# Optimization experiments

Measured on AMD Instinct MI355X. Metric: run time of the kernel, lower is better.

The kernel has to match this reference:

```python
import jax, jax.numpy as jnp
import numpy as np

BN_EPS = 1e-5

def _gin_mlp(h, wa, ba, wb, bb):
    # 2-layer MLP: Linear -> ReLU -> Linear
    return jax.nn.relu(h @ wa + ba) @ wb + bb

def _gin_conv(x, src, dst, n, wa, ba, wb, bb):
    # GIN aggregation: (1+eps)*x + sum_{j->i} x_j, eps=0 (PyG default)
    agg = jax.ops.segment_sum(x[src], dst, num_segments=n)
    return _gin_mlp(x + agg, wa, ba, wb, bb)

def _batchnorm(h, gamma, beta):
    # track_running_stats=False -> always batch stats, biased variance
    mean = jnp.mean(h, axis=0)
    var = jnp.var(h, axis=0)
    return (h - mean) * jax.lax.rsqrt(var + BN_EPS) * gamma + beta

def setup_inputs() -> dict:
    key = jax.random.key(0)
    ks = jax.random.split(key, 8)
    N, E, F, H, C = 100000, 1600000, 64, 64, 10
    s = 0.05
    return {
        "x": jax.random.normal(ks[0], (N, F), dtype=jnp.float32),
        "edge_index": jax.random.randint(ks[1], (2, E), 0, N, dtype=jnp.int64),
        "w1a": jax.random.normal(ks[2], (F, H), dtype=jnp.float32) * s,
        "b1a": jnp.zeros((H,), jnp.float32),
        "w1b": jax.random.normal(ks[3], (H, H), dtype=jnp.float32) * s,
        "b1b": jnp.zeros((H,), jnp.float32),
        "bn_gamma": jnp.ones((H,), jnp.float32),
        "bn_beta": jnp.zeros((H,), jnp.float32),
        "w2a": jax.random.normal(ks[4], (H, H), dtype=jnp.float32) * s,
        "b2a": jnp.zeros((H,), jnp.float32),
        "w2b": jax.random.normal(ks[5], (H, H), dtype=jnp.float32) * s,
        "b2b": jnp.zeros((H,), jnp.float32),
        "lin_w": jax.random.normal(ks[6], (H, C), dtype=jnp.float32) * s,
        "lin_b": jnp.zeros((C,), jnp.float32),
    }

def reference(x, edge_index, w1a, b1a, w1b, b1b, bn_gamma, bn_beta,
              w2a, b2a, w2b, b2b, lin_w, lin_b):
    n = x.shape[0]
    src, dst = edge_index[0], edge_index[1]
    h1 = _gin_conv(x, src, dst, n, w1a, b1a, w1b, b1b)   # [N, H]
    h1 = _batchnorm(h1, bn_gamma, bn_beta)               # relu1 never applied (faithful)
    h2 = _gin_conv(h1, src, dst, n, w2a, b2a, w2b, b2b)  # [N, H]
    return h2 @ lin_w + lin_b                            # [N, C]
```

## Files before the change

kernel.cpp:

```cpp
#include <hip/hip_runtime.h>
#include <hip/hip_fp16.h>

#define H 64
#define CBS 512
#define CB_BITS 9
#define TILE 8192
#define CAP 9216
#define NSTAT 64
#define RPK_BLKS 53

typedef _Float16 f16;
typedef __attribute__((ext_vector_type(8))) _Float16 v8h;
typedef __attribute__((ext_vector_type(4))) float v4f;

__global__ __launch_bounds__(256)
void init_kernel(int* __restrict__ gcursor, float* __restrict__ statsR, int CB) {
    int t = threadIdx.x;
    if (t < CB) gcursor[t * 16] = t * CAP;
    for (int i = t; i < NSTAT * 128; i += 256) statsR[i] = 0.f;
}

__global__ __launch_bounds__(256)
void front_kernel(const int* __restrict__ ei, int* __restrict__ gcursor,
                  int* __restrict__ pairs, int E, int N, int CB, int ntiles,
                  const float* __restrict__ x, f16* __restrict__ xh, int total4,
                  const float* __restrict__ W1a, const float* __restrict__ W1b,
                  const float* __restrict__ W2a, const float* __restrict__ W2b,
                  const float* __restrict__ B2b, const float* __restrict__ LW,
                  const float* __restrict__ LB,
                  f16* __restrict__ pk1a, f16* __restrict__ pk1b,
                  f16* __restrict__ pk2a, f16* __restrict__ pkf,
                  float* __restrict__ bf) {
    __shared__ int sd[256];
    __shared__ int excl[256];
    __shared__ int gbase[256];
    __shared__ int lcur[256];
    __shared__ int stage[TILE];
    __shared__ unsigned char bin8[TILE];
    int b = blockIdx.x;
    int t = threadIdx.x;

    if (b < ntiles) {
        int base = b * TILE;
        int cnt = min(TILE, E - base);
        sd[t] = 0;
        __syncthreads();
        for (int i = t; i < cnt; i += 256) {
            int s = ei[base + i];
            int d = ei[E + base + i];
            if ((unsigned)s < (unsigned)N && (unsigned)d < (unsigned)N)
                atomicAdd(&sd[d >> CB_BITS], 1);
        }
        __syncthreads();
        int v = sd[t];
        __syncthreads();
        for (int off = 1; off < 256; off <<= 1) {
            int add = (t >= off) ? sd[t - off] : 0;
            __syncthreads();
            sd[t] += add;
            __syncthreads();
        }
        int ex = sd[t] - v;
        excl[t] = ex;
        lcur[t] = ex;
        if (t < CB && v > 0) gbase[t] = atomicAdd(&gcursor[t * 16], v);
        int tot = sd[255];
        __syncthreads();
        for (int i = t; i < cnt; i += 256) {
            int s = ei[base + i];
            int d = ei[E + base + i];
            if ((unsigned)s < (unsigned)N && (unsigned)d < (unsigned)N) {
                int cb = d >> CB_BITS;
                int pos = atomicAdd(&lcur[cb], 1);
                stage[pos] = s | ((d & (CBS - 1)) << 17);
                bin8[pos] = (unsigned char)cb;
            }
        }
        __syncthreads();
        for (int i = t; i < tot; i += 256) {
            int b8 = bin8[i];
            pairs[gbase[b8] + (i - excl[b8])] = stage[i];
        }
        return;
    }
    b -= ntiles;
    if (b < RPK_BLKS) {
        int tt = b * 256 + t;
        if (tt < 12288) {
            int m = tt >> 12;
            int e = tt & 4095;
            int j = e & 7, lane = (e >> 3) & 63, ks = (e >> 9) & 1, nt = e >> 10;
            int row = ks * 32 + ((lane >> 4) & 3) * 8 + j;
            int col = nt * 16 + (lane & 15);
            const float* W = (m == 0) ? W1a : (m == 1) ? W1b : W2a;
            f16* P = (m == 0) ? pk1a : (m == 1) ? pk1b : pk2a;
            P[e] = (f16)W[row * 64 + col];
        } else if (tt < 13312) {
            int e = tt - 12288;
            int j = e & 7, lane = (e >> 3) & 63, ks = e >> 9;
            int row = ks * 32 + ((lane >> 4) & 3) * 8 + j;
            int col = lane & 15;
            float a = 0.f;
            if (col < 10)
                for (int m = 0; m < H; ++m) a = fmaf(W2b[row * 64 + m], LW[m * 10 + col], a);
            pkf[e] = (f16)a;
        } else if (tt < 13322) {
            int c = tt - 13312;
            float a = LB[c];
            for (int m = 0; m < H; ++m) a = fmaf(B2b[m], LW[m * 10 + c], a);
            bf[c] = a;
        }
        return;
    }
    b -= RPK_BLKS;
    int i = b * 256 + t;
    if (i >= total4) return;
    float4 v = ((const float4*)x)[i];
    f16 h0 = (f16)v.x, h1 = (f16)v.y, h2 = (f16)v.z, h3 = (f16)v.w;
    ushort4 pk;
    pk.x = *(unsigned short*)&h0; pk.y = *(unsigned short*)&h1;
    pk.z = *(unsigned short*)&h2; pk.w = *(unsigned short*)&h3;
    ((ushort4*)xh)[i] = pk;
}

__global__ __launch_bounds__(256)
void bucket_csr_kernel(const int* __restrict__ pairs, const int* __restrict__ gcursor,
                       int* __restrict__ ebuf, int* __restrict__ rowptr, int N, int CB) {
    __shared__ int hist[CBS];
    __shared__ int cur[CBS];
    __shared__ int sd[256];
    __shared__ int carry_s;
    int b = blockIdx.x;
    int t = threadIdx.x;
    int c_t = (t < CB) ? (gcursor[t * 16] - t * CAP) : 0;
    sd[t] = c_t; __syncthreads();
    for (int off = 1; off < 256; off <<= 1) {
        int add = (t >= off) ? sd[t - off] : 0;
        __syncthreads();
        sd[t] += add;
        __syncthreads();
    }
    int cnt = gcursor[b * 16] - b * CAP;
    int gb = sd[b] - cnt;
    if (b == 0 && t == 0) rowptr[N] = sd[255];
    __syncthreads();

    int pb = b * CAP;
    for (int i = t; i < CBS; i += 256) hist[i] = 0;
    if (t == 0) carry_s = 0;
    __syncthreads();
    for (int i = t; i < cnt; i += 256)
        atomicAdd(&hist[(pairs[pb + i] >> 17) & (CBS - 1)], 1);
    __syncthreads();
    for (int start = 0; start < CBS; start += 256) {
        int v = hist[start + t];
        sd[t] = v; __syncthreads();
        for (int off = 1; off < 256; off <<= 1) {
            int add = (t >= off) ? sd[t - off] : 0;
            __syncthreads();
            sd[t] += add;
            __syncthreads();
        }
        int ex = sd[t] - v + carry_s;
        cur[start + t] = ex;
        int node = b * CBS + start + t;
        if (node < N) rowptr[node] = gb + ex;
        __syncthreads();
        if (t == 0) carry_s += sd[255];
        __syncthreads();
    }
    for (int i = t; i < cnt; i += 256) {
        int p = pairs[pb + i];
        int pos = atomicAdd(&cur[(p >> 17) & (CBS - 1)], 1);
        ebuf[gb + pos] = p & 0x1FFFF;
    }
}

__global__ __launch_bounds__(256)
void gather1_kernel(const f16* __restrict__ xh, const int* __restrict__ rowptr,
                    const int* __restrict__ ebuf, f16* __restrict__ bufA,
                    int N, int Em1) {
    int wid = (int)(((long long)blockIdx.x * blockDim.x + threadIdx.x) >> 6);
    int lane = threadIdx.x & 63;
    int g = lane >> 3, fl = lane & 7;
    int node = wid * 8 + g;
    bool vn = node < N;
    int p0 = 0, deg = 0;
    if (vn) {
        p0 = rowptr[node];
        deg = rowptr[node + 1] - p0;
    }
    float a[8];
    {
        v8h s = {};
        if (vn) s = *(const v8h*)(xh + ((size_t)node << 6) + fl * 8);
#pragma unroll
        for (int j = 0; j < 8; ++j) a[j] = (float)s[j];
    }
    int k = 0;
    for (; k + 8 <= deg; k += 8) {
        int idx[8];
#pragma unroll
        for (int q = 0; q < 8; ++q) idx[q] = ebuf[p0 + k + q];
#pragma unroll
        for (int q = 0; q < 8; ++q) {
            v8h v = *(const v8h*)(xh + ((size_t)idx[q] << 6) + fl * 8);
#pragma unroll
            for (int j = 0; j < 8; ++j) a[j] += (float)v[j];
        }
    }
    if (k < deg) {
        int idx[8];
#pragma unroll
        for (int q = 0; q < 8; ++q) idx[q] = ebuf[min(p0 + k + q, Em1)];
#pragma unroll
        for (int q = 0; q < 8; ++q) {
            if (k + q < deg) {
                v8h v = *(const v8h*)(xh + ((size_t)idx[q] << 6) + fl * 8);
#pragma unroll
                for (int j = 0; j < 8; ++j) a[j] += (float)v[j];
            }
        }
    }
    if (vn) {
        v8h o;
#pragma unroll
        for (int j = 0; j < 8; ++j) o[j] = (f16)a[j];
        *(v8h*)(bufA + ((size_t)node << 6) + fl * 8) = o;
    }
}

__global__ __launch_bounds__(256)
void gather2_kernel(const f16* __restrict__ h1p, const float* __restrict__ scale,
                    const float* __restrict__ shiftv, const int* __restrict__ rowptr,
                    const int* __restrict__ ebuf, f16* __restrict__ bufC,
                    int N, int Em1) {
    int wid = (int)(((long long)blockIdx.x * blockDim.x + threadIdx.x) >> 6);
    int lane = threadIdx.x & 63;
    int g = lane >> 3, fl = lane & 7;
    int node = wid * 8 + g;
    bool vn = node < N;
    int p0 = 0, deg = 0;
    if (vn) {
        p0 = rowptr[node];
        deg = rowptr[node + 1] - p0;
    }
    float a[8];
    {
        v8h s = {};
        if (vn) s = *(const v8h*)(h1p + ((size_t)node << 6) + fl * 8);
#pragma unroll
        for (int j = 0; j < 8; ++j) a[j] = (float)s[j];
    }
    int k = 0;
    for (; k + 8 <= deg; k += 8) {
        int idx[8];
#pragma unroll
        for (int q = 0; q < 8; ++q) idx[q] = ebuf[p0 + k + q];
#pragma unroll
        for (int q = 0; q < 8; ++q) {
            v8h v = *(const v8h*)(h1p + ((size_t)idx[q] << 6) + fl * 8);
#pragma unroll
            for (int j = 0; j < 8; ++j) a[j] += (float)v[j];
        }
    }
    if (k < deg) {
        int idx[8];
#pragma unroll
        for (int q = 0; q < 8; ++q) idx[q] = ebuf[min(p0 + k + q, Em1)];
#pragma unroll
        for (int q = 0; q < 8; ++q) {
            if (k + q < deg) {
                v8h v = *(const v8h*)(h1p + ((size_t)idx[q] << 6) + fl * 8);
#pragma unroll
                for (int j = 0; j < 8; ++j) a[j] += (float)v[j];
            }
        }
    }
    if (vn) {
        float4 s0 = *(const float4*)(scale + fl * 8);
        float4 s1 = *(const float4*)(scale + fl * 8 + 4);
        float4 h0 = *(const float4*)(shiftv + fl * 8);
        float4 h1 = *(const float4*)(shiftv + fl * 8 + 4);
        float degp1 = (float)(deg + 1);
        float sc[8] = {s0.x, s0.y, s0.z, s0.w, s1.x, s1.y, s1.z, s1.w};
        float sh[8] = {h0.x, h0.y, h0.z, h0.w, h1.x, h1.y, h1.z, h1.w};
        v8h o;
#pragma unroll
        for (int j = 0; j < 8; ++j) o[j] = (f16)(a[j] * sc[j] + degp1 * sh[j]);
        *(v8h*)(bufC + ((size_t)node << 6) + fl * 8) = o;
    }
}

__global__ __launch_bounds__(256)
void mlp1_kernel(const f16* __restrict__ bufA, f16* __restrict__ h1p,
                 const f16* __restrict__ pk1a, const f16* __restrict__ pk1b,
                 const float* __restrict__ B1a, const float* __restrict__ B1b,
                 float* __restrict__ statsR, int N) {
    __shared__ f16 Su[4][16 * 72];
    __shared__ f16 Sh[4][16 * 72];
    __shared__ float red[2][4][64];
    int t = threadIdx.x, wv = t >> 6, lane = t & 63;
    int quad = lane >> 4, r16 = lane & 15;
    int node0 = blockIdx.x * 64 + wv * 16;
    int nodeA = node0 + r16;

    v8h a0 = {}, a1 = {};
    if (nodeA < N) {
        a0 = *(const v8h*)(bufA + (size_t)nodeA * 64 + quad * 8);
        a1 = *(const v8h*)(bufA + (size_t)nodeA * 64 + 32 + quad * 8);
    }
#pragma unroll
    for (int nt = 0; nt < 4; ++nt) {
        v8h b0 = *(const v8h*)(pk1a + (((nt * 2 + 0) * 64 + lane) << 3));
        v8h b1 = *(const v8h*)(pk1a + (((nt * 2 + 1) * 64 + lane) << 3));
        v4f c = {0.f, 0.f, 0.f, 0.f};
        c = __builtin_amdgcn_mfma_f32_16x16x32_f16(a0, b0, c, 0, 0, 0);
        c = __builtin_amdgcn_mfma_f32_16x16x32_f16(a1, b1, c, 0, 0, 0);
        float bias = B1a[nt * 16 + r16];
#pragma unroll
        for (int reg = 0; reg < 4; ++reg)
            Su[wv][(quad * 4 + reg) * 72 + nt * 16 + r16] = (f16)fmaxf(c[reg] + bias, 0.f);
    }
    __syncthreads();
    v8h u0 = *(const v8h*)(&Su[wv][r16 * 72 + quad * 8]);
    v8h u1 = *(const v8h*)(&Su[wv][r16 * 72 + 32 + quad * 8]);
#pragma unroll
    for (int nt = 0; nt < 4; ++nt) {
        v8h b0 = *(const v8h*)(pk1b + (((nt * 2 + 0) * 64 + lane) << 3));
        v8h b1 = *(const v8h*)(pk1b + (((nt * 2 + 1) * 64 + lane) << 3));
        v4f c = {0.f, 0.f, 0.f, 0.f};
        c = __builtin_amdgcn_mfma_f32_16x16x32_f16(u0, b0, c, 0, 0, 0);
        c = __builtin_amdgcn_mfma_f32_16x16x32_f16(u1, b1, c, 0, 0, 0);
        float bias = B1b[nt * 16 + r16];
#pragma unroll
        for (int reg = 0; reg < 4; ++reg) {
            int row = quad * 4 + reg;
            bool valid = (node0 + row) < N;
            Sh[wv][row * 72 + nt * 16 + r16] = valid ? (f16)(c[reg] + bias) : (f16)0;
        }
    }
    __syncthreads();
    for (int i = lane; i < 1024; i += 64) {
        int row = i >> 6, col = i & 63;
        int node = node0 + row;
        if (node < N) h1p[(size_t)node * 64 + col] = Sh[wv][row * 72 + col];
    }
    float s = 0.f, s2 = 0.f;
#pragma unroll
    for (int row = 0; row < 16; ++row) {
        float v = (float)Sh[wv][row * 72 + lane];
        s += v;
        s2 = fmaf(v, v, s2);
    }
    red[0][wv][lane] = s;
    red[1][wv][lane] = s2;
    __syncthreads();
    if (wv == 0) {
        float ts  = (red[0][0][lane] + red[0][1][lane]) + (red[0][2][lane] + red[0][3][lane]);
        float ts2 = (red[1][0][lane] + red[1][1][lane]) + (red[1][2][lane] + red[1][3][lane]);
        float* st = statsR + (size_t)(blockIdx.x & (NSTAT - 1)) * 128;
        unsafeAtomicAdd(&st[lane], ts);
        unsafeAtomicAdd(&st[64 + lane], ts2);
    }
}

__global__ void bn_finalize_kernel(const float* __restrict__ statsR,
                                   const float* __restrict__ gamma,
                                   const float* __restrict__ beta,
                                   float* __restrict__ scale, float* __restrict__ shiftv, float n) {
    int f = threadIdx.x;
    if (f >= H) return;
    float s = 0.f, s2 = 0.f;
    for (int r = 0; r < NSTAT; ++r) {
        s  += statsR[r * 128 + f];
        s2 += statsR[r * 128 + 64 + f];
    }
    float mean = s / n;
    float var = s2 / n - mean * mean;
    var = fmaxf(var, 0.f);
    float sc = gamma[f] * rsqrtf(var + 1e-5f);
    scale[f] = sc;
    shiftv[f] = beta[f] - mean * sc;
}

__global__ __launch_bounds__(256)
void mlp2_kernel(const f16* __restrict__ bufC,
                 const f16* __restrict__ pk2a, const f16* __restrict__ pkf,
                 const float* __restrict__ B2a, const float* __restrict__ bf,
                 float* __restrict__ out, int N) {
    __shared__ f16 Su[4][16 * 72];
    int t = threadIdx.x, wv = t >> 6, lane = t & 63;
    int quad = lane >> 4, r16 = lane & 15;
    int node0 = blockIdx.x * 64 + wv * 16;
    int nodeA = node0 + r16;

    v8h a0 = {}, a1 = {};
    if (nodeA < N) {
        a0 = *(const v8h*)(bufC + (size_t)nodeA * 64 + quad * 8);
        a1 = *(const v8h*)(bufC + (size_t)nodeA * 64 + 32 + quad * 8);
    }
#pragma unroll
    for (int nt = 0; nt < 4; ++nt) {
        v8h b0 = *(const v8h*)(pk2a + (((nt * 2 + 0) * 64 + lane) << 3));
        v8h b1 = *(const v8h*)(pk2a + (((nt * 2 + 1) * 64 + lane) << 3));
        v4f c = {0.f, 0.f, 0.f, 0.f};
        c = __builtin_amdgcn_mfma_f32_16x16x32_f16(a0, b0, c, 0, 0, 0);
        c = __builtin_amdgcn_mfma_f32_16x16x32_f16(a1, b1, c, 0, 0, 0);
        float bias = B2a[nt * 16 + r16];
#pragma unroll
        for (int reg = 0; reg < 4; ++reg)
            Su[wv][(quad * 4 + reg) * 72 + nt * 16 + r16] = (f16)fmaxf(c[reg] + bias, 0.f);
    }
    __syncthreads();
    v8h u0 = *(const v8h*)(&Su[wv][r16 * 72 + quad * 8]);
    v8h u1 = *(const v8h*)(&Su[wv][r16 * 72 + 32 + quad * 8]);
    v8h b0 = *(const v8h*)(pkf + ((0 * 64 + lane) << 3));
    v8h b1 = *(const v8h*)(pkf + ((1 * 64 + lane) << 3));
    v4f c = {0.f, 0.f, 0.f, 0.f};
    c = __builtin_amdgcn_mfma_f32_16x16x32_f16(u0, b0, c, 0, 0, 0);
    c = __builtin_amdgcn_mfma_f32_16x16x32_f16(u1, b1, c, 0, 0, 0);
    if (r16 < 10) {
        float bias = bf[r16];
#pragma unroll
        for (int reg = 0; reg < 4; ++reg) {
            int node = node0 + quad * 4 + reg;
            if (node < N) out[(size_t)node * 10 + r16] = c[reg] + bias;
        }
    }
}

extern "C" void kernel_launch(void* const* d_in, const int* in_sizes, int n_in,
                              void* d_out, int out_size, void* d_ws, size_t ws_size,
                              hipStream_t stream) {
    const float* x    = (const float*)d_in[0];
    const int*   ei   = (const int*)d_in[1];
    const float* w1a  = (const float*)d_in[2];
    const float* b1a  = (const float*)d_in[3];
    const float* w1b  = (const float*)d_in[4];
    const float* b1b  = (const float*)d_in[5];
    const float* bng  = (const float*)d_in[6];
    const float* bnb  = (const float*)d_in[7];
    const float* w2a  = (const float*)d_in[8];
    const float* b2a  = (const float*)d_in[9];
    const float* w2b  = (const float*)d_in[10];
    const float* b2b  = (const float*)d_in[11];
    const float* linw = (const float*)d_in[12];
    const float* linb = (const float*)d_in[13];

    int N = in_sizes[0] / H;
    int E = in_sizes[1] / 2;
    int CB = (N + CBS - 1) / CBS;

    size_t NH = (size_t)N * H;
    char*  wsb    = (char*)d_ws;
    f16*   xh     = (f16*)wsb;
    f16*   bufA   = (f16*)(wsb + NH * 2);
    f16*   bufC   = (f16*)(wsb + NH * 4);
    float* stats  = (float*)(wsb + NH * 6);
    float* scale  = stats + 128;
    float* shiftv = stats + 192;
    float* bf     = stats + 256;
    f16*   pk1a   = (f16*)(bf + 16);
    f16*   pk1b   = pk1a + 4096;
    f16*   pk2a   = pk1b + 4096;
    f16*   pkf    = pk2a + 4096;
    int*   gcursor= (int*)(pkf + 1024);
    int*   rowptr = gcursor + 256 * 16;
    int*   ebuf   = rowptr + (N + 1);
    int*   pairs  = ebuf + E;
    float* statsR = (float*)(pairs + (size_t)CB * CAP);

    int ntiles = (E + TILE - 1) / TILE;
    int total4 = (int)(NH / 4);
    int cvtblocks = (total4 + 255) / 256;
    int mblocks = (N + 63) / 64;
    int nwaves = (N + 7) / 8;
    int gblocks = (int)(((long long)nwaves * 64 + 255) / 256);

    init_kernel<<<1, 256, 0, stream>>>(gcursor, statsR, CB);
    front_kernel<<<ntiles + RPK_BLKS + cvtblocks, 256, 0, stream>>>(
        ei, gcursor, pairs, E, N, CB, ntiles,
        x, xh, total4,
        w1a, w1b, w2a, w2b, b2b, linw, linb,
        pk1a, pk1b, pk2a, pkf, bf);
    bucket_csr_kernel<<<CB, 256, 0, stream>>>(pairs, gcursor, ebuf, rowptr, N, CB);

    gather1_kernel<<<gblocks, 256, 0, stream>>>(xh, rowptr, ebuf, bufA, N, E - 1);
    mlp1_kernel<<<mblocks, 256, 0, stream>>>(bufA, bufA, pk1a, pk1b, b1a, b1b, statsR, N);
    bn_finalize_kernel<<<1, 64, 0, stream>>>(statsR, bng, bnb, scale, shiftv, (float)N);

    gather2_kernel<<<gblocks, 256, 0, stream>>>(bufA, scale, shiftv, rowptr, ebuf, bufC, N, E - 1);
    mlp2_kernel<<<mblocks, 256, 0, stream>>>(bufC, pk2a, pkf, b2a, bf, (float*)d_out, N);
}
```

Measured before the change: 232.4 us.

## Prefetch edge indices in gathers, fold BN finalize into gather2, halve front tile

```diff
diff --git a/kernel.cpp b/kernel.cpp
--- a/kernel.cpp
+++ b/kernel.cpp
@@ -4,7 +4,7 @@
 #define H 64
 #define CBS 512
 #define CB_BITS 9
-#define TILE 8192
+#define TILE 4096
 #define CAP 9216
 #define NSTAT 64
 #define RPK_BLKS 53
@@ -198,16 +198,41 @@
         for (int j = 0; j < 8; ++j) a[j] = (float)s[j];
     }
     int k = 0;
-    for (; k + 8 <= deg; k += 8) {
-        int idx[8];
-#pragma unroll
-        for (int q = 0; q < 8; ++q) idx[q] = ebuf[p0 + k + q];
+    if (deg >= 16) {
+        int idxA[8];
+#pragma unroll
+        for (int q = 0; q < 8; ++q) idxA[q] = ebuf[p0 + q];
+        for (; k + 16 <= deg; k += 8) {
+            int idxB[8];
+#pragma unroll
+            for (int q = 0; q < 8; ++q) idxB[q] = ebuf[p0 + k + 8 + q];
+#pragma unroll
+            for (int q = 0; q < 8; ++q) {
+                v8h v = *(const v8h*)(xh + ((size_t)idxA[q] << 6) + fl * 8);
+#pragma unroll
+                for (int j = 0; j < 8; ++j) a[j] += (float)v[j];
+            }
+#pragma unroll
+            for (int q = 0; q < 8; ++q) idxA[q] = idxB[q];
+        }
 #pragma unroll
         for (int q = 0; q < 8; ++q) {
-            v8h v = *(const v8h*)(xh + ((size_t)idx[q] << 6) + fl * 8);
+            v8h v = *(const v8h*)(xh + ((size_t)idxA[q] << 6) + fl * 8);
 #pragma unroll
             for (int j = 0; j < 8; ++j) a[j] += (float)v[j];
         }
+        k += 8;
+    } else if (deg >= 8) {
+        int idxA[8];
+#pragma unroll
+        for (int q = 0; q < 8; ++q) idxA[q] = ebuf[p0 + q];
+#pragma unroll
+        for (int q = 0; q < 8; ++q) {
+            v8h v = *(const v8h*)(xh + ((size_t)idxA[q] << 6) + fl * 8);
+#pragma unroll
+            for (int j = 0; j < 8; ++j) a[j] += (float)v[j];
+        }
+        k = 8;
     }
     if (k < deg) {
         int idx[8];
@@ -231,12 +256,30 @@
 }
 
 __global__ __launch_bounds__(256)
-void gather2_kernel(const f16* __restrict__ h1p, const float* __restrict__ scale,
-                    const float* __restrict__ shiftv, const int* __restrict__ rowptr,
-                    const int* __restrict__ ebuf, f16* __restrict__ bufC,
-                    int N, int Em1) {
-    int wid = (int)(((long long)blockIdx.x * blockDim.x + threadIdx.x) >> 6);
-    int lane = threadIdx.x & 63;
+void gather2_kernel(const f16* __restrict__ h1p, const float* __restrict__ statsR,
+                    const float* __restrict__ gamma, const float* __restrict__ beta,
+                    const int* __restrict__ rowptr, const int* __restrict__ ebuf,
+                    f16* __restrict__ bufC, int N, int Em1, float n) {
+    __shared__ float s_scale[64];
+    __shared__ float s_shift[64];
+    int t = threadIdx.x;
+    if (t < 64) {
+        float s = 0.f, s2 = 0.f;
+#pragma unroll 8
+        for (int r = 0; r < NSTAT; ++r) {
+            s  += statsR[r * 128 + t];
+            s2 += statsR[r * 128 + 64 + t];
+        }
+        float mean = s / n;
+        float var = fmaxf(s2 / n - mean * mean, 0.f);
+        float sc = gamma[t] * rsqrtf(var + 1e-5f);
+        s_scale[t] = sc;
+        s_shift[t] = beta[t] - mean * sc;
+    }
+    __syncthreads();
+
+    int wid = (int)(((long long)blockIdx.x * blockDim.x + t) >> 6);
+    int lane = t & 63;
     int g = lane >> 3, fl = lane & 7;
     int node = wid * 8 + g;
     bool vn = node < N;
@@ -253,16 +296,41 @@
         for (int j = 0; j < 8; ++j) a[j] = (float)s[j];
     }
     int k = 0;
-    for (; k + 8 <= deg; k += 8) {
-        int idx[8];
-#pragma unroll
-        for (int q = 0; q < 8; ++q) idx[q] = ebuf[p0 + k + q];
+    if (deg >= 16) {
+        int idxA[8];
+#pragma unroll
+        for (int q = 0; q < 8; ++q) idxA[q] = ebuf[p0 + q];
+        for (; k + 16 <= deg; k += 8) {
+            int idxB[8];
+#pragma unroll
+            for (int q = 0; q < 8; ++q) idxB[q] = ebuf[p0 + k + 8 + q];
+#pragma unroll
+            for (int q = 0; q < 8; ++q) {
+                v8h v = *(const v8h*)(h1p + ((size_t)idxA[q] << 6) + fl * 8);
+#pragma unroll
+                for (int j = 0; j < 8; ++j) a[j] += (float)v[j];
+            }
+#pragma unroll
+            for (int q = 0; q < 8; ++q) idxA[q] = idxB[q];
+        }
 #pragma unroll
         for (int q = 0; q < 8; ++q) {
-            v8h v = *(const v8h*)(h1p + ((size_t)idx[q] << 6) + fl * 8);
+            v8h v = *(const v8h*)(h1p + ((size_t)idxA[q] << 6) + fl * 8);
 #pragma unroll
             for (int j = 0; j < 8; ++j) a[j] += (float)v[j];
         }
+        k += 8;
+    } else if (deg >= 8) {
+        int idxA[8];
+#pragma unroll
+        for (int q = 0; q < 8; ++q) idxA[q] = ebuf[p0 + q];
+#pragma unroll
+        for (int q = 0; q < 8; ++q) {
+            v8h v = *(const v8h*)(h1p + ((size_t)idxA[q] << 6) + fl * 8);
+#pragma unroll
+            for (int j = 0; j < 8; ++j) a[j] += (float)v[j];
+        }
+        k = 8;
     }
     if (k < deg) {
         int idx[8];
@@ -278,16 +346,11 @@
         }
     }
     if (vn) {
-        float4 s0 = *(const float4*)(scale + fl * 8);
-        float4 s1 = *(const float4*)(scale + fl * 8 + 4);
-        float4 h0 = *(const float4*)(shiftv + fl * 8);
-        float4 h1 = *(const float4*)(shiftv + fl * 8 + 4);
         float degp1 = (float)(deg + 1);
-        float sc[8] = {s0.x, s0.y, s0.z, s0.w, s1.x, s1.y, s1.z, s1.w};
-        float sh[8] = {h0.x, h0.y, h0.z, h0.w, h1.x, h1.y, h1.z, h1.w};
         v8h o;
 #pragma unroll
-        for (int j = 0; j < 8; ++j) o[j] = (f16)(a[j] * sc[j] + degp1 * sh[j]);
+        for (int j = 0; j < 8; ++j)
+            o[j] = (f16)(a[j] * s_scale[fl * 8 + j] + degp1 * s_shift[fl * 8 + j]);
         *(v8h*)(bufC + ((size_t)node << 6) + fl * 8) = o;
     }
 }
@@ -363,25 +426,6 @@
         unsafeAtomicAdd(&st[lane], ts);
         unsafeAtomicAdd(&st[64 + lane], ts2);
     }
-}
-
-__global__ void bn_finalize_kernel(const float* __restrict__ statsR,
-                                   const float* __restrict__ gamma,
-                                   const float* __restrict__ beta,
-                                   float* __restrict__ scale, float* __restrict__ shiftv, float n) {
-    int f = threadIdx.x;
-    if (f >= H) return;
-    float s = 0.f, s2 = 0.f;
-    for (int r = 0; r < NSTAT; ++r) {
-        s  += statsR[r * 128 + f];
-        s2 += statsR[r * 128 + 64 + f];
-    }
-    float mean = s / n;
-    float var = s2 / n - mean * mean;
-    var = fmaxf(var, 0.f);
-    float sc = gamma[f] * rsqrtf(var + 1e-5f);
-    scale[f] = sc;
-    shiftv[f] = beta[f] - mean * sc;
 }
 
 __global__ __launch_bounds__(256)
@@ -488,8 +532,8 @@
 
     gather1_kernel<<<gblocks, 256, 0, stream>>>(xh, rowptr, ebuf, bufA, N, E - 1);
     mlp1_kernel<<<mblocks, 256, 0, stream>>>(bufA, bufA, pk1a, pk1b, b1a, b1b, statsR, N);
-    bn_finalize_kernel<<<1, 64, 0, stream>>>(statsR, bng, bnb, scale, shiftv, (float)N);
-
-    gather2_kernel<<<gblocks, 256, 0, stream>>>(bufA, scale, shiftv, rowptr, ebuf, bufC, N, E - 1);
+
+    gather2_kernel<<<gblocks, 256, 0, stream>>>(
+        bufA, statsR, bng, bnb, rowptr, ebuf, bufC, N, E - 1, (float)N);
     mlp2_kernel<<<mblocks, 256, 0, stream>>>(bufC, pk2a, pkf, b2a, bf, (float*)d_out, N);
 }
```

Result: no change. 230.7 us (-0.7%).
